# Performance work log

Measured on AMD Instinct MI355X. Metric: run time of the kernel, lower is better.

Reference implementation:

```python
import jax, jax.numpy as jnp
import numpy as np

NUM_CAPS = 8
NITER = 3
TAU = 1.0
N_NODES = 50000
N_EDGES = 800000
D_FEAT = 128


def _l2norm(v):
    # matches torch fn.normalize(dim=-1, eps=1e-12): v / max(||v||, eps)
    n = jnp.linalg.norm(v, axis=-1, keepdims=True)
    return v / jnp.maximum(n, 1e-12)


def setup_inputs() -> dict:
    key = jax.random.key(0)
    k1, k2, k3 = jax.random.split(key, 3)
    x = jax.random.normal(k1, (N_NODES, D_FEAT), dtype=jnp.float32)
    src = jax.random.randint(k2, (N_EDGES,), 0, N_NODES)
    trg = jax.random.randint(k3, (N_EDGES,), 0, N_NODES)
    edge_index = jnp.stack([src, trg], axis=0).astype(jnp.int64)
    return {"x": x, "edge_index": edge_index}


def reference(x, edge_index):
    num_node, num_dim = x.shape
    dpc = num_dim // NUM_CAPS  # dim per capsule
    src, trg = edge_index[0], edge_index[1]

    xc = _l2norm(x.reshape(num_node, NUM_CAPS, dpc))  # [N, C, d]
    z = xc[src]                                        # [E, C, d] gathered source caps
    u = xc
    for _ in range(NITER):
        # per-edge, per-capsule agreement score
        p = jnp.einsum('ecd,ecd->ec', z, u[trg])       # [E, C]
        p = jax.nn.softmax(p / TAU, axis=1)
        msg = z * p[:, :, None]                        # [E, C, d]
        u = jax.ops.segment_sum(msg, trg, num_segments=num_node)  # [N, C, d]
        u = _l2norm(u + xc)
    return u.reshape(num_node, num_dim)
```

## Files before the change

kernel.cpp:

```cpp
#include <hip/hip_runtime.h>
#include <hip/hip_bf16.h>

#define DF   128
#define DPC  16
#define WPB  4
#define EPT  4
#define KCAP 62
#define RWRD 32

__device__ __forceinline__ float cap_sum(float v) {
    v += __shfl_xor(v, 1);
    v += __shfl_xor(v, 2);
    v += __shfl_xor(v, 4);
    return v;
}
__device__ __forceinline__ float bits_lo(unsigned int w) {
    union { unsigned int u; float f; } c; c.u = w << 16; return c.f;
}
__device__ __forceinline__ float bits_hi(unsigned int w) {
    union { unsigned int u; float f; } c; c.u = w & 0xFFFF0000u; return c.f;
}
__device__ __forceinline__ unsigned int f2b_pack(float lo, float hi) {
    __hip_bfloat16 a = __float2bfloat16(lo), b = __float2bfloat16(hi);
    unsigned short ua = *reinterpret_cast<unsigned short*>(&a);
    unsigned short ub = *reinterpret_cast<unsigned short*>(&b);
    return ((unsigned int)ub << 16) | ua;
}
__device__ __forceinline__ float2 load_x2(const void* __restrict__ xraw, int fp32,
                                          int node, int lane) {
    size_t off = (size_t)node * DF + (size_t)lane * 2;
    if (fp32) {
        return *reinterpret_cast<const float2*>((const float*)xraw + off);
    } else {
        unsigned int w = ((const unsigned int*)xraw)[(size_t)node * 64 + lane];
        return make_float2(bits_lo(w), bits_hi(w));
    }
}
__device__ __forceinline__ int2 edge_st(const int* __restrict__ ei, int i64,
                                        int e, int n_edges) {
    size_t si = i64 ? (size_t)2 * e             : (size_t)e;
    size_t ti = i64 ? (size_t)2 * (n_edges + e) : (size_t)(n_edges + e);
    return make_int2(ei[si], ei[ti]);
}
__device__ __forceinline__ void cvt16(const uint4& w0, const uint4& w1, float* z) {
    z[0]  = bits_lo(w0.x); z[1]  = bits_hi(w0.x);
    z[2]  = bits_lo(w0.y); z[3]  = bits_hi(w0.y);
    z[4]  = bits_lo(w0.z); z[5]  = bits_hi(w0.z);
    z[6]  = bits_lo(w0.w); z[7]  = bits_hi(w0.w);
    z[8]  = bits_lo(w1.x); z[9]  = bits_hi(w1.x);
    z[10] = bits_lo(w1.y); z[11] = bits_hi(w1.y);
    z[12] = bits_lo(w1.z); z[13] = bits_hi(w1.z);
    z[14] = bits_lo(w1.w); z[15] = bits_hi(w1.w);
}
__device__ __forceinline__ void proc_chunk(const uint4& w0, const uint4& w1,
                                           bool valid, const float* u, float* acc) {
    float z[DPC];
    cvt16(w0, w1, z);
    float p = 0.0f;
    #pragma unroll
    for (int j = 0; j < DPC; ++j) p = fmaf(z[j], u[j], p);
    float ex = __expf(p);
    float sd = ex;
    sd += __shfl_xor(sd, 1);
    sd += __shfl_xor(sd, 2);
    sd += __shfl_xor(sd, 4);
    float w = valid ? ex * __builtin_amdgcn_rcpf(sd) : 0.0f;
    #pragma unroll
    for (int j = 0; j < DPC; ++j) acc[j] = fmaf(w, z[j], acc[j]);
}

__global__ void k_detect_zero(const unsigned int* __restrict__ xw,
                              const unsigned int* __restrict__ ew,
                              int* __restrict__ flags, int* __restrict__ bkt,
                              int n_nodes) {
    if (blockIdx.x == 0) {
        __shared__ int s_nan, s_zero;
        int tid = threadIdx.x;
        if (tid == 0) { s_nan = 0; s_zero = 0; }
        __syncthreads();
        int cnt_nan = 0;
        for (int i = tid; i < 4096; i += 256) {
            unsigned int lo = xw[i] & 0xFFFFu;
            if ((lo & 0x7F80u) == 0x7F80u) cnt_nan++;
        }
        int cnt_zero = 0;
        for (int i = tid; i < 1024; i += 256) {
            if (ew[2 * i + 1] == 0u) cnt_zero++;
        }
        atomicAdd(&s_nan, cnt_nan);
        atomicAdd(&s_zero, cnt_zero);
        __syncthreads();
        if (tid == 0) {
            flags[0] = (s_nan > 0) ? 1 : 0;
            flags[1] = (s_zero > 512) ? 1 : 0;
        }
    } else {
        int i = (blockIdx.x - 1) * 256 + threadIdx.x;
        if (i < n_nodes) bkt[(size_t)i * RWRD] = 0;
    }
}

__global__ void k_prep(const void* __restrict__ xraw, unsigned int* __restrict__ xcb,
                       const int* __restrict__ ei, int* __restrict__ bkt,
                       const int* __restrict__ flags,
                       int n_nodes, int n_edges, int nb_bucket) {
    const int fp32 = flags[0];
    int wid  = (blockIdx.x * blockDim.x + threadIdx.x) >> 6;
    int lane = threadIdx.x & 63;
    if (wid < n_nodes) {
        float2 v = load_x2(xraw, fp32, wid, lane);
        float ss = cap_sum(v.x * v.x + v.y * v.y);
        float scale = 1.0f / fmaxf(sqrtf(ss), 1e-12f);
        int c = lane >> 3, jp = lane & 7;
        int w = (jp < 4) ? (c * 4 + jp) : (32 + c * 4 + (jp - 4));
        xcb[(size_t)wid * 64 + w] = f2b_pack(v.x * scale, v.y * scale);
    }
    if (blockIdx.x < (unsigned)nb_bucket) {
        const int i64 = flags[1];
        int base = blockIdx.x * (256 * EPT) + threadIdx.x;
        int s[EPT], t[EPT], slot[EPT];
        bool ok[EPT];
        #pragma unroll
        for (int k = 0; k < EPT; ++k) {
            int e = base + k * 256;
            if (e < n_edges) {
                int2 st = edge_st(ei, i64, e, n_edges);
                s[k] = st.x; t[k] = st.y;
                ok[k] = (unsigned)st.x < (unsigned)n_nodes &&
                        (unsigned)st.y < (unsigned)n_nodes;
            } else ok[k] = false;
        }
        #pragma unroll
        for (int k = 0; k < EPT; ++k)
            if (ok[k]) slot[k] = atomicAdd(&bkt[(size_t)t[k] * RWRD], 1);
        #pragma unroll
        for (int k = 0; k < EPT; ++k)
            if (ok[k] && slot[k] < KCAP)
                ((unsigned short*)&bkt[(size_t)t[k] * RWRD])[2 + slot[k]] =
                    (unsigned short)s[k];
    }
}

__global__ void k_route(const int* __restrict__ bkt,
                        const unsigned int* __restrict__ xcb,
                        float* __restrict__ u_out, int n_nodes) {
    int t    = (blockIdx.x * blockDim.x + threadIdx.x) >> 6;
    int lane = threadIdx.x & 63;
    if (t >= n_nodes) return;
    const int e8 = lane >> 3;
    const int c  = lane & 7;
    const int coff = c * 16;
    const char* __restrict__ xb = (const char*)xcb;

    const int* __restrict__ row = bkt + (size_t)t * RWRD;
    int deg = __builtin_amdgcn_readfirstlane(row[0]);
    deg = min(deg, KCAP);
    const unsigned short* __restrict__ erow = (const unsigned short*)row + 2;

    float xt[DPC];
    {
        size_t trow = (size_t)t << 8;
        uint4 t0 = *reinterpret_cast<const uint4*>(xb + trow + coff);
        uint4 t1 = *reinterpret_cast<const uint4*>(xb + trow + 128 + coff);
        cvt16(t0, t1, xt);
    }
    float ss = 0.0f;
    #pragma unroll
    for (int j = 0; j < DPC; ++j) ss = fmaf(xt[j], xt[j], ss);
    float sc = __builtin_amdgcn_rsqf(fmaxf(ss, 1e-24f));
    float u[DPC];
    #pragma unroll
    for (int j = 0; j < DPC; ++j) { xt[j] *= sc; u[j] = xt[j]; }

    uint4 cw0, cw1;
    if (deg > 0) {
        int off0 = ((int)erow[e8 < deg ? e8 : 0]) << 8;
        cw0 = *reinterpret_cast<const uint4*>(xb + off0 + coff);
        cw1 = *reinterpret_cast<const uint4*>(xb + off0 + 128 + coff);
    }

    for (int it = 0; it < 3; ++it) {
        float acc[DPC];
        #pragma unroll
        for (int j = 0; j < DPC; ++j) acc[j] = 0.0f;

        for (int base = 0; base < deg; base += 8) {
            uint4 nw0, nw1;
            bool havenext = (base + 8 < deg);
            bool pf = havenext || (it < 2);
            if (pf) {
                int ni = (havenext ? base + 8 : 0) + e8;
                int offn = ((int)erow[ni < deg ? ni : 0]) << 8;
                nw0 = *reinterpret_cast<const uint4*>(xb + offn + coff);
                nw1 = *reinterpret_cast<const uint4*>(xb + offn + 128 + coff);
            }
            proc_chunk(cw0, cw1, (base + e8) < deg, u, acc);
            if (pf) { cw0 = nw0; cw1 = nw1; }
        }
        #pragma unroll
        for (int j = 0; j < DPC; ++j) {
            acc[j] += __shfl_xor(acc[j], 8);
            acc[j] += __shfl_xor(acc[j], 16);
            acc[j] += __shfl_xor(acc[j], 32);
        }
        float s2 = 0.0f;
        #pragma unroll
        for (int j = 0; j < DPC; ++j) {
            u[j] = acc[j] + xt[j];
            s2 = fmaf(u[j], u[j], s2);
        }
        float sc2 = __builtin_amdgcn_rsqf(fmaxf(s2, 1e-24f));
        #pragma unroll
        for (int j = 0; j < DPC; ++j) u[j] *= sc2;
    }

    if (e8 == 0) {
        float* dst = u_out + (size_t)t * DF + c * DPC;
        #pragma unroll
        for (int j = 0; j < DPC; j += 4)
            *reinterpret_cast<float4*>(dst + j) =
                make_float4(u[j], u[j+1], u[j+2], u[j+3]);
    }
}

extern "C" void kernel_launch(void* const* d_in, const int* in_sizes, int n_in,
                              void* d_out, int out_size, void* d_ws, size_t ws_size,
                              hipStream_t stream) {
    const void* x  = d_in[0];
    const int*  ei = (const int*)d_in[1];
    const int n_nodes = in_sizes[0] / DF;
    const int n_edges = in_sizes[1] / 2;
    const size_t NC = (size_t)n_nodes * DF;

    unsigned int* xcb = (unsigned int*)d_ws;
    int* bkt   = (int*)(xcb + NC / 2);
    int* flags = bkt + (size_t)n_nodes * RWRD;

    float* u_out = (float*)d_out;

    const int tpb = 64 * WPB;
    const int nb_nodes  = (n_nodes + WPB - 1) / WPB;
    const int nb_zero   = (n_nodes + 255) / 256 + 1;
    const int nb_bucket = (n_edges + 256 * EPT - 1) / (256 * EPT);

    k_detect_zero<<<nb_zero, 256, 0, stream>>>(
        (const unsigned int*)x, (const unsigned int*)ei, flags, bkt, n_nodes);
    k_prep<<<nb_nodes, tpb, 0, stream>>>(x, xcb, ei, bkt, flags,
                                         n_nodes, n_edges, nb_bucket);
    k_route<<<nb_nodes, tpb, 0, stream>>>(bkt, xcb, u_out, n_nodes);
}
```

Before: 225.5 us.

## Keep first three neighbor chunks in registers across routing iterations

The routing kernel now loads each node's whole bucket row with one coalesced read per lane and pulls neighbor ids out through shuffles instead of issuing scalar loads. The first 24 neighbor capsule rows stay in registers for all three iterations rather than being gathered again on every pass; only neighbors past 24 are reloaded. The zeroing kernel now clears the full bucket rows with 16-byte stores instead of only the count word. This adds zeroing traffic and register pressure, which may lower occupancy.

```diff
diff --git a/kernel.cpp b/kernel.cpp
--- a/kernel.cpp
+++ b/kernel.cpp
@@ -96,7 +96,10 @@
         }
     } else {
         int i = (blockIdx.x - 1) * 256 + threadIdx.x;
-        if (i < n_nodes) bkt[(size_t)i * RWRD] = 0;
+        int total = n_nodes * (RWRD / 4);
+        if (i < total) {
+            reinterpret_cast<uint4*>(bkt)[i] = make_uint4(0u, 0u, 0u, 0u);
+        }
     }
 }
 
@@ -152,51 +155,58 @@
     const int coff = c * 16;
     const char* __restrict__ xb = (const char*)xcb;
 
-    const int* __restrict__ row = bkt + (size_t)t * RWRD;
-    int deg = __builtin_amdgcn_readfirstlane(row[0]);
+    unsigned rw = ((const unsigned*)(bkt + (size_t)t * RWRD))[lane & 31];
+
+    size_t trow = (size_t)t << 8;
+    uint4 t0 = *reinterpret_cast<const uint4*>(xb + trow + coff);
+    uint4 t1 = *reinterpret_cast<const uint4*>(xb + trow + 128 + coff);
+
+    int deg = __builtin_amdgcn_readfirstlane((int)rw);
     deg = min(deg, KCAP);
-    const unsigned short* __restrict__ erow = (const unsigned short*)row + 2;
-
-    float xt[DPC];
-    {
-        size_t trow = (size_t)t << 8;
-        uint4 t0 = *reinterpret_cast<const uint4*>(xb + trow + coff);
-        uint4 t1 = *reinterpret_cast<const uint4*>(xb + trow + 128 + coff);
-        cvt16(t0, t1, xt);
-    }
+
+    auto nid = [&](int s) -> int {
+        int g = 4 + 2 * s;
+        unsigned wv = __shfl(rw, (lane & 32) | (g >> 2));
+        return (int)((g & 2) ? (wv >> 16) : (wv & 0xFFFFu));
+    };
+    auto ldc = [&](int k, uint4& a, uint4& b) {
+        int s  = e8 + 8 * k;
+        int sl = (s < deg) ? s : 0;
+        int off = nid(sl) << 8;
+        a = *reinterpret_cast<const uint4*>(xb + off + coff);
+        b = *reinterpret_cast<const uint4*>(xb + off + 128 + coff);
+    };
+
+    uint4 k0a, k0b, k1a, k1b, k2a, k2b;
+    if (deg > 0)  ldc(0, k0a, k0b);
+    if (deg > 8)  ldc(1, k1a, k1b);
+    if (deg > 16) ldc(2, k2a, k2b);
+
+    float xt[DPC], u[DPC];
+    cvt16(t0, t1, xt);
     float ss = 0.0f;
     #pragma unroll
     for (int j = 0; j < DPC; ++j) ss = fmaf(xt[j], xt[j], ss);
     float sc = __builtin_amdgcn_rsqf(fmaxf(ss, 1e-24f));
-    float u[DPC];
     #pragma unroll
     for (int j = 0; j < DPC; ++j) { xt[j] *= sc; u[j] = xt[j]; }
-
-    uint4 cw0, cw1;
-    if (deg > 0) {
-        int off0 = ((int)erow[e8 < deg ? e8 : 0]) << 8;
-        cw0 = *reinterpret_cast<const uint4*>(xb + off0 + coff);
-        cw1 = *reinterpret_cast<const uint4*>(xb + off0 + 128 + coff);
-    }
 
     for (int it = 0; it < 3; ++it) {
         float acc[DPC];
         #pragma unroll
         for (int j = 0; j < DPC; ++j) acc[j] = 0.0f;
 
-        for (int base = 0; base < deg; base += 8) {
-            uint4 nw0, nw1;
-            bool havenext = (base + 8 < deg);
-            bool pf = havenext || (it < 2);
-            if (pf) {
-                int ni = (havenext ? base + 8 : 0) + e8;
-                int offn = ((int)erow[ni < deg ? ni : 0]) << 8;
-                nw0 = *reinterpret_cast<const uint4*>(xb + offn + coff);
-                nw1 = *reinterpret_cast<const uint4*>(xb + offn + 128 + coff);
+        if (deg > 0)  proc_chunk(k0a, k0b, e8 < deg,      u, acc);
+        if (deg > 8)  proc_chunk(k1a, k1b, 8  + e8 < deg, u, acc);
+        if (deg > 16) proc_chunk(k2a, k2b, 16 + e8 < deg, u, acc);
+        if (deg > 24) {
+            for (int base = 24; base < deg; base += 8) {
+                uint4 a, b;
+                ldc(base >> 3, a, b);
+                proc_chunk(a, b, base + e8 < deg, u, acc);
             }
-            proc_chunk(cw0, cw1, (base + e8) < deg, u, acc);
-            if (pf) { cw0 = nw0; cw1 = nw1; }
-        }
+        }
+
         #pragma unroll
         for (int j = 0; j < DPC; ++j) {
             acc[j] += __shfl_xor(acc[j], 8);
@@ -240,7 +250,7 @@
 
     const int tpb = 64 * WPB;
     const int nb_nodes  = (n_nodes + WPB - 1) / WPB;
-    const int nb_zero   = (n_nodes + 255) / 256 + 1;
+    const int nb_zero   = (n_nodes * (RWRD / 4) + 255) / 256 + 1;
     const int nb_bucket = (n_edges + 256 * EPT - 1) / (256 * EPT);
 
     k_detect_zero<<<nb_zero, 256, 0, stream>>>(
```

Result: no change. 225.7 us (+0.1%).
